# Kernel optimization log

Hardware: AMD Instinct MI355X
Metric: run time of the kernel (lower is better)

The kernel has to match this reference:

```python
import jax, jax.numpy as jnp
import numpy as np
from functools import partial

TOP_K = 2
LN_EPS = 1e-5


def setup_inputs() -> dict:
    key = jax.random.key(0)
    ks = jax.random.split(key, 4)
    B, T, H, F, E = 2, 2048, 1024, 4096, 8
    hidden_states = jax.random.normal(ks[0], (B, T, H), dtype=jnp.float32)
    # Router weights: original inits to zeros; use small random so routing is non-degenerate.
    router_w = jax.random.normal(ks[1], (E, H), dtype=jnp.float32) * 0.02
    router_b = jnp.zeros((E,), dtype=jnp.float32)
    W1 = jax.random.normal(ks[2], (E, H, F), dtype=jnp.float32) * (1.0 / np.sqrt(H))
    b1 = jnp.zeros((E, F), dtype=jnp.float32)
    W2 = jax.random.normal(ks[3], (E, F, H), dtype=jnp.float32) * (1.0 / np.sqrt(F))
    b2 = jnp.zeros((E, H), dtype=jnp.float32)
    ln_gamma = jnp.ones((H,), dtype=jnp.float32)
    ln_beta = jnp.zeros((H,), dtype=jnp.float32)
    return {"hidden_states": hidden_states, "router_w": router_w, "router_b": router_b,
            "W1": W1, "b1": b1, "W2": W2, "b2": b2,
            "ln_gamma": ln_gamma, "ln_beta": ln_beta}


def _layer_norm(x, gamma, beta):
    mu = jnp.mean(x, axis=-1, keepdims=True)
    var = jnp.var(x, axis=-1, keepdims=True)
    return (x - mu) * jax.lax.rsqrt(var + LN_EPS) * gamma + beta


def _moe_forward(hidden_states, router_w, router_b, W1, b1, W2, b2, ln_gamma, ln_beta):
    B, T, H = hidden_states.shape
    E = router_w.shape[0]
    N = B * T
    x = hidden_states.reshape(N, H)
    # Router (jitter=0.0, eval mode): logits [N, E]
    logits = x @ router_w.T + router_b
    topk_vals, topk_idx = jax.lax.top_k(logits, TOP_K)        # [N, K]
    topk_w = jax.nn.softmax(topk_vals, axis=-1)               # [N, K]
    # Scatter top-k weights into a dense combine matrix [N, E] (zeros elsewhere).
    probs = jnp.zeros((N, E), dtype=x.dtype).at[jnp.arange(N)[:, None], topk_idx].set(topk_w)
    # Per-expert FFN via scan over the (small, fixed) expert axis; each step is one
    # big GEMM over all tokens weighted by that expert's combine prob (0 for
    # tokens not routed to it) — same math as gather/MLP/scatter with no capacity drop.
    def body(acc, params_e):
        Wa, ba, Wb, bb, pe = params_e          # pe: [N]
        h = jax.nn.gelu(x @ Wa + ba, approximate=False)   # [N, F]
        y = h @ Wb + bb                                    # [N, H]
        return acc + y * pe[:, None], None
    out, _ = jax.lax.scan(body, jnp.zeros_like(x), (W1, b1, W2, b2, probs.T))
    out = out.reshape(B, T, H)
    return _layer_norm(out + hidden_states, ln_gamma, ln_beta)


def reference(hidden_states, router_w, router_b, W1, b1, W2, b2, ln_gamma, ln_beta):
    return _moe_forward(hidden_states, router_w, router_b, W1, b1, W2, b2, ln_gamma, ln_beta)
```

## Files before the change

kernel.cpp:

```cpp
#include <hip/hip_runtime.h>
#include <hip/hip_bf16.h>


typedef unsigned short u16;
typedef unsigned int u32;
typedef __attribute__((ext_vector_type(4))) float f32x4;
typedef __attribute__((ext_vector_type(8))) short s16x8;
typedef __attribute__((ext_vector_type(8))) unsigned short u16x8;

#define GLD16(gp, lp) __builtin_amdgcn_global_load_lds( \
    (const __attribute__((address_space(1))) void*)(gp), \
    (__attribute__((address_space(3))) void*)(lp), 16, 0, 0)

__device__ __forceinline__ u16 f2bf(float f) {
    union { float f; u32 u; } v; v.f = f;
    u32 u = v.u;
    return (u16)((u + 0x7fffu + ((u >> 16) & 1u)) >> 16);
}

__device__ __forceinline__ float gelu_f(float v) {
    const float u = v * (0.7978845608f + 0.0356774081f * v * v);
    const float t = __expf(-2.0f * u);
    return v * __builtin_amdgcn_rcpf(1.0f + t);
}

__global__ void k_init(int* cc) { if (threadIdx.x < 16) cc[threadIdx.x] = 0; }

__global__ __launch_bounds__(256) void k_router(
    const float* __restrict__ x, const float* __restrict__ rw, const float* __restrict__ rb,
    u16* __restrict__ xb, int* __restrict__ eidx, float* __restrict__ wgt, int* __restrict__ counts)
{
    const int wav = threadIdx.x >> 6, lane = threadIdx.x & 63;
    const int t = blockIdx.x * 4 + wav;
    const float* xt = x + (size_t)t * 1024;
    float acc[8] = {0.f,0.f,0.f,0.f,0.f,0.f,0.f,0.f};
    #pragma unroll
    for (int c = 0; c < 4; c++) {
        const int base = c * 256 + lane * 4;
        const float4 xv = *(const float4*)(xt + base);
        ushort4 pk;
        pk.x = f2bf(xv.x); pk.y = f2bf(xv.y); pk.z = f2bf(xv.z); pk.w = f2bf(xv.w);
        *(ushort4*)(xb + (size_t)t * 1024 + base) = pk;
        #pragma unroll
        for (int e = 0; e < 8; e++) {
            const float4 wv = *(const float4*)(rw + e * 1024 + base);
            acc[e] += xv.x * wv.x + xv.y * wv.y + xv.z * wv.z + xv.w * wv.w;
        }
    }
    #pragma unroll
    for (int e = 0; e < 8; e++) {
        #pragma unroll
        for (int s = 32; s; s >>= 1) acc[e] += __shfl_xor(acc[e], s);
    }
    if (lane == 0) {
        float v0 = -3e38f, v1 = -3e38f; int i0 = 0, i1 = 0;
        #pragma unroll
        for (int e = 0; e < 8; e++) {
            const float l = acc[e] + rb[e];
            if (l > v0) { v1 = v0; i1 = i0; v0 = l; i0 = e; }
            else if (l > v1) { v1 = l; i1 = e; }
        }
        const float w0 = 1.0f / (1.0f + expf(v1 - v0));
        eidx[2 * t] = i0; eidx[2 * t + 1] = i1;
        wgt[2 * t] = w0; wgt[2 * t + 1] = 1.0f - w0;
        atomicAdd(&counts[i0], 1); atomicAdd(&counts[i1], 1);
    }
}

__global__ void k_offsets(const int* __restrict__ counts, int* __restrict__ offsets) {
    if (threadIdx.x == 0) {
        int s = 0;
        for (int e = 0; e < 8; e++) { offsets[e] = s; s += counts[e]; }
        offsets[8] = s;
    }
}

__global__ __launch_bounds__(256) void k_place(
    const int* __restrict__ eidx, const int* __restrict__ offsets, int* __restrict__ cursors,
    int* __restrict__ rows, int* __restrict__ pos_of)
{
    const int a = blockIdx.x * 256 + threadIdx.x;
    const int e = eidx[a];
    const int pos = offsets[e] + atomicAdd(&cursors[e], 1);
    rows[pos] = a >> 1;
    pos_of[a] = pos;
}

__global__ __launch_bounds__(256) void k_transp(
    const float* __restrict__ src, u16* __restrict__ dst, int R, int C)
{
    const int e = blockIdx.z;
    const float* s = src + (size_t)e * R * C;
    u16* d = dst + (size_t)e * R * C;
    const int c = blockIdx.x * 64 + (threadIdx.x >> 2);
    const int r0 = blockIdx.y * 32 + (threadIdx.x & 3) * 8;
    u16x8 v;
    #pragma unroll
    for (int k = 0; k < 8; k++)
        v[k] = f2bf(s[(size_t)(r0 + k) * C + c]);
    *(u16x8*)(d + (size_t)c * R + r0) = v;
}

__global__ __launch_bounds__(256, 4) void k_gemm1(
    const u16* __restrict__ xb, const u16* __restrict__ W1t, const float* __restrict__ b1,
    u16* __restrict__ hbuf, const int* __restrict__ rows, const int* __restrict__ offsets)
{
    const int fid = blockIdx.x;
    const int swz = (fid & 7) * 1024 + (fid >> 3);
    const int y = swz & 31, xx = (swz >> 5) & 31, e = swz >> 10;

    const int off = offsets[e], cnt = offsets[e + 1] - off;
    const int row0 = y * 128;
    if (row0 >= cnt) return;
    const int n0 = xx * 128;
    const int tid = threadIdx.x;
    const int lane = tid & 63, wav = tid >> 6;

    __shared__ u16 At[2][128][32];
    __shared__ u16 Bt[2][128][32];

    const int ar0 = tid >> 2, ar1 = ar0 + 64;
    const int cl8 = (tid & 3) * 8;
    const int t0 = rows[off + min(row0 + ar0, cnt - 1)];
    const int t1 = rows[off + min(row0 + ar1, cnt - 1)];
    const u16* a_src0 = xb + (size_t)t0 * 1024 + cl8;
    const u16* a_src1 = xb + (size_t)t1 * 1024 + cl8;
    const u16* b_src0 = W1t + ((size_t)e * 4096 + n0 + ar0) * 1024 + cl8;
    const u16* b_src1 = W1t + ((size_t)e * 4096 + n0 + ar1) * 1024 + cl8;

    f32x4 acc[4][4] = {};
    const int wr = wav >> 1, wc = wav & 1;
    const int koff = (lane >> 4) * 8;
    const u16* Ab = &At[0][wr * 64 + (lane & 15)][koff];
    const u16* Bb = &Bt[0][wc * 64 + (lane & 15)][koff];

    #define STAGE1(b, k0) { \
        char* ad = (char*)At + (b) * 8192 + wav * 1024; \
        char* bd = (char*)Bt + (b) * 8192 + wav * 1024; \
        GLD16(a_src0 + (k0), ad); \
        GLD16(a_src1 + (k0), ad + 4096); \
        GLD16(b_src0 + (k0), bd); \
        GLD16(b_src1 + (k0), bd + 4096); }

    #define COMPUTE1(b) { \
        const u16* Abp = Ab + (b) * 4096; \
        const u16* Bbp = Bb + (b) * 4096; \
        s16x8 af[4], bfr[4]; \
        _Pragma("unroll") \
        for (int i = 0; i < 4; i++) { \
            af[i]  = *(const s16x8*)(Abp + i * 512); \
            bfr[i] = *(const s16x8*)(Bbp + i * 512); \
        } \
        _Pragma("unroll") \
        for (int mi = 0; mi < 4; mi++) \
            _Pragma("unroll") \
            for (int ni = 0; ni < 4; ni++) \
                acc[mi][ni] = __builtin_amdgcn_mfma_f32_16x16x32_bf16(af[mi], bfr[ni], acc[mi][ni], 0, 0, 0); }

    int b = 0;
    STAGE1(0, 0);
    __syncthreads();
    for (int k0 = 32; k0 < 1024; k0 += 32) {
        STAGE1(b ^ 1, k0);
        COMPUTE1(b);
        __syncthreads();
        b ^= 1;
    }
    COMPUTE1(b);

    const int rb4 = (lane >> 4) * 4;
    const int colbase = n0 + wc * 64 + (lane & 15);
    float bias[4];
    #pragma unroll
    for (int ni = 0; ni < 4; ni++) bias[ni] = b1[e * 4096 + colbase + ni * 16];
    #pragma unroll
    for (int mi = 0; mi < 4; mi++) {
        #pragma unroll
        for (int j = 0; j < 4; j++) {
            const int lrow = wr * 64 + mi * 16 + rb4 + j;
            if (row0 + lrow < cnt) {
                const size_t gr = (size_t)(off + row0 + lrow);
                #pragma unroll
                for (int ni = 0; ni < 4; ni++) {
                    const float v = acc[mi][ni][j] + bias[ni];
                    hbuf[gr * 4096 + colbase + ni * 16] = f2bf(gelu_f(v));
                }
            }
        }
    }
}

__global__ __launch_bounds__(256, 4) void k_gemm2(
    const u16* __restrict__ hbuf, const u16* __restrict__ W2t, const float* __restrict__ b2,
    float* __restrict__ y0, float* __restrict__ y1, const int* __restrict__ offsets)
{
    const int fid = blockIdx.x;
    const int swz = (fid & 7) * 512 + (fid >> 3);
    const int y = swz & 31, xx = (swz >> 5) & 7, z = swz >> 8;
    const int e = z >> 1, kh = z & 1;

    const int off = offsets[e], cnt = offsets[e + 1] - off;
    const int row0 = y * 128;
    if (row0 >= cnt) return;
    const int n0 = xx * 128;
    const int tid = threadIdx.x;
    const int lane = tid & 63, wav = tid >> 6;
    const int kbase = kh * 2048;

    __shared__ u16 At[2][128][32];
    __shared__ u16 Bt[2][128][32];

    const int ar0 = tid >> 2, ar1 = ar0 + 64;
    const int cl8 = (tid & 3) * 8;
    const u16* a_src0 = hbuf + (size_t)(off + min(row0 + ar0, cnt - 1)) * 4096 + kbase + cl8;
    const u16* a_src1 = hbuf + (size_t)(off + min(row0 + ar1, cnt - 1)) * 4096 + kbase + cl8;
    const u16* b_src0 = W2t + ((size_t)e * 1024 + n0 + ar0) * 4096 + kbase + cl8;
    const u16* b_src1 = W2t + ((size_t)e * 1024 + n0 + ar1) * 4096 + kbase + cl8;

    f32x4 acc[4][4] = {};
    const int wr = wav >> 1, wc = wav & 1;
    const int koff = (lane >> 4) * 8;
    const u16* Ab = &At[0][wr * 64 + (lane & 15)][koff];
    const u16* Bb = &Bt[0][wc * 64 + (lane & 15)][koff];

    int b = 0;
    STAGE1(0, 0);
    __syncthreads();
    for (int k0 = 32; k0 < 2048; k0 += 32) {
        STAGE1(b ^ 1, k0);
        COMPUTE1(b);
        __syncthreads();
        b ^= 1;
    }
    COMPUTE1(b);

    float* yy = kh ? y1 : y0;
    const int rb4 = (lane >> 4) * 4;
    const int colbase = n0 + wc * 64 + (lane & 15);
    float bias[4];
    #pragma unroll
    for (int ni = 0; ni < 4; ni++) bias[ni] = kh ? 0.f : b2[e * 1024 + colbase + ni * 16];
    #pragma unroll
    for (int mi = 0; mi < 4; mi++) {
        #pragma unroll
        for (int j = 0; j < 4; j++) {
            const int lrow = wr * 64 + mi * 16 + rb4 + j;
            if (row0 + lrow < cnt) {
                const size_t gr = (size_t)(off + row0 + lrow);
                #pragma unroll
                for (int ni = 0; ni < 4; ni++)
                    yy[gr * 1024 + colbase + ni * 16] = acc[mi][ni][j] + bias[ni];
            }
        }
    }
}

__global__ __launch_bounds__(256) void k_combine(
    const float* __restrict__ x, const float* __restrict__ y0, const float* __restrict__ y1,
    const int* __restrict__ pos_of, const float* __restrict__ wgt,
    const float* __restrict__ gamma, const float* __restrict__ beta,
    float* __restrict__ out)
{
    const int t = blockIdx.x;
    const int tid = threadIdx.x;
    const int p0 = pos_of[2 * t], p1 = pos_of[2 * t + 1];
    const float w0 = wgt[2 * t], w1 = wgt[2 * t + 1];
    const int j4 = tid * 4;
    const float4 xv = *(const float4*)(x + (size_t)t * 1024 + j4);
    const float4 ya0 = *(const float4*)(y0 + (size_t)p0 * 1024 + j4);
    const float4 yb0 = *(const float4*)(y1 + (size_t)p0 * 1024 + j4);
    const float4 ya1 = *(const float4*)(y0 + (size_t)p1 * 1024 + j4);
    const float4 yb1 = *(const float4*)(y1 + (size_t)p1 * 1024 + j4);
    float a0 = xv.x + w0 * (ya0.x + yb0.x) + w1 * (ya1.x + yb1.x);
    float a1 = xv.y + w0 * (ya0.y + yb0.y) + w1 * (ya1.y + yb1.y);
    float a2 = xv.z + w0 * (ya0.z + yb0.z) + w1 * (ya1.z + yb1.z);
    float a3 = xv.w + w0 * (ya0.w + yb0.w) + w1 * (ya1.w + yb1.w);
    float s = a0 + a1 + a2 + a3;
    float q = a0 * a0 + a1 * a1 + a2 * a2 + a3 * a3;
    #pragma unroll
    for (int o = 32; o; o >>= 1) { s += __shfl_xor(s, o); q += __shfl_xor(q, o); }
    __shared__ float ls[4], lq[4];
    const int wav = tid >> 6, lane = tid & 63;
    if (lane == 0) { ls[wav] = s; lq[wav] = q; }
    __syncthreads();
    s = ls[0] + ls[1] + ls[2] + ls[3];
    q = lq[0] + lq[1] + lq[2] + lq[3];
    const float mu = s * (1.0f / 1024.0f);
    const float var = q * (1.0f / 1024.0f) - mu * mu;
    const float rs = rsqrtf(var + 1e-5f);
    const float4 g = *(const float4*)(gamma + j4);
    const float4 b = *(const float4*)(beta + j4);
    float4 o4;
    o4.x = (a0 - mu) * rs * g.x + b.x;
    o4.y = (a1 - mu) * rs * g.y + b.y;
    o4.z = (a2 - mu) * rs * g.z + b.z;
    o4.w = (a3 - mu) * rs * g.w + b.w;
    *(float4*)(out + (size_t)t * 1024 + j4) = o4;
}

extern "C" void kernel_launch(void* const* d_in, const int* in_sizes, int n_in,
                              void* d_out, int out_size, void* d_ws, size_t ws_size,
                              hipStream_t stream) {
    const float* x     = (const float*)d_in[0];
    const float* rw    = (const float*)d_in[1];
    const float* rb    = (const float*)d_in[2];
    const float* W1    = (const float*)d_in[3];
    const float* b1    = (const float*)d_in[4];
    const float* W2    = (const float*)d_in[5];
    const float* b2    = (const float*)d_in[6];
    const float* gamma = (const float*)d_in[7];
    const float* beta  = (const float*)d_in[8];
    float* out = (float*)d_out;

    char* p = (char*)d_ws;
    auto alloc = [&](size_t bytes) { char* r = p; p += (bytes + 255) & ~(size_t)255; return r; };
    int*   counts  = (int*)alloc(16 * sizeof(int));
    int*   cursors = counts + 8;
    int*   offsets = (int*)alloc(9 * sizeof(int));
    int*   eidx    = (int*)alloc(8192 * sizeof(int));
    float* wgt     = (float*)alloc(8192 * sizeof(float));
    int*   pos_of  = (int*)alloc(8192 * sizeof(int));
    int*   rows    = (int*)alloc(8192 * sizeof(int));
    u16*   xb      = (u16*)alloc((size_t)4096 * 1024 * 2);
    u16*   W1t     = (u16*)alloc((size_t)8 * 4096 * 1024 * 2);
    u16*   W2t     = (u16*)alloc((size_t)8 * 1024 * 4096 * 2);
    u16*   hbuf    = (u16*)alloc((size_t)8192 * 4096 * 2);
    float* y0 = (float*)W1t;
    float* y1 = y0 + (size_t)8192 * 1024;

    hipLaunchKernelGGL(k_init, dim3(1), dim3(64), 0, stream, counts);
    hipLaunchKernelGGL(k_router, dim3(1024), dim3(256), 0, stream, x, rw, rb, xb, eidx, wgt, counts);
    hipLaunchKernelGGL(k_offsets, dim3(1), dim3(64), 0, stream, counts, offsets);
    hipLaunchKernelGGL(k_place, dim3(32), dim3(256), 0, stream, eidx, offsets, cursors, rows, pos_of);
    hipLaunchKernelGGL(k_transp, dim3(64, 32, 8), dim3(256), 0, stream, W1, W1t, 1024, 4096);
    hipLaunchKernelGGL(k_transp, dim3(16, 128, 8), dim3(256), 0, stream, W2, W2t, 4096, 1024);
    hipLaunchKernelGGL(k_gemm1, dim3(8192), dim3(256), 0, stream, xb, W1t, b1, hbuf, rows, offsets);
    hipLaunchKernelGGL(k_gemm2, dim3(4096), dim3(256), 0, stream, hbuf, W2t, b2, y0, y1, offsets);
    hipLaunchKernelGGL(k_combine, dim3(4096), dim3(256), 0, stream, x, y0, y1, pos_of, wgt, gamma, beta, out);
}
```

Measured before the change: 477.6 us.

## Fuse weight fp32-to-bf16 transpose into GEMM tile loads, drop transpose kernels

Removes the two standalone weight transpose/convert kernels. Each GEMM now loads fp32 weights directly, converts them to bf16 in registers and writes them transposed into padded LDS (stride 40). The A and B tiles switch from async global-to-LDS loads to register-staged loads, and occupancy drops to 3 blocks. This avoids a full pass writing and rereading the bf16 weight copies, but each GEMM tile now reads fp32 weights (twice the bytes), and those weights are re-read across the many token tiles per expert.

```diff
diff --git a/kernel.cpp b/kernel.cpp
--- a/kernel.cpp
+++ b/kernel.cpp
@@ -8,9 +8,7 @@
 typedef __attribute__((ext_vector_type(8))) short s16x8;
 typedef __attribute__((ext_vector_type(8))) unsigned short u16x8;
 
-#define GLD16(gp, lp) __builtin_amdgcn_global_load_lds( \
-    (const __attribute__((address_space(1))) void*)(gp), \
-    (__attribute__((address_space(3))) void*)(lp), 16, 0, 0)
+#define LDSTR 40
 
 __device__ __forceinline__ u16 f2bf(float f) {
     union { float f; u32 u; } v; v.f = f;
@@ -86,23 +84,8 @@
     pos_of[a] = pos;
 }
 
-__global__ __launch_bounds__(256) void k_transp(
-    const float* __restrict__ src, u16* __restrict__ dst, int R, int C)
-{
-    const int e = blockIdx.z;
-    const float* s = src + (size_t)e * R * C;
-    u16* d = dst + (size_t)e * R * C;
-    const int c = blockIdx.x * 64 + (threadIdx.x >> 2);
-    const int r0 = blockIdx.y * 32 + (threadIdx.x & 3) * 8;
-    u16x8 v;
-    #pragma unroll
-    for (int k = 0; k < 8; k++)
-        v[k] = f2bf(s[(size_t)(r0 + k) * C + c]);
-    *(u16x8*)(d + (size_t)c * R + r0) = v;
-}
-
-__global__ __launch_bounds__(256, 4) void k_gemm1(
-    const u16* __restrict__ xb, const u16* __restrict__ W1t, const float* __restrict__ b1,
+__global__ __launch_bounds__(256, 3) void k_gemm1(
+    const u16* __restrict__ xb, const float* __restrict__ W1, const float* __restrict__ b1,
     u16* __restrict__ hbuf, const int* __restrict__ rows, const int* __restrict__ offsets)
 {
     const int fid = blockIdx.x;
@@ -114,62 +97,75 @@
     if (row0 >= cnt) return;
     const int n0 = xx * 128;
     const int tid = threadIdx.x;
-    const int lane = tid & 63, wav = tid >> 6;
-
-    __shared__ u16 At[2][128][32];
-    __shared__ u16 Bt[2][128][32];
-
-    const int ar0 = tid >> 2, ar1 = ar0 + 64;
-    const int cl8 = (tid & 3) * 8;
-    const int t0 = rows[off + min(row0 + ar0, cnt - 1)];
-    const int t1 = rows[off + min(row0 + ar1, cnt - 1)];
-    const u16* a_src0 = xb + (size_t)t0 * 1024 + cl8;
-    const u16* a_src1 = xb + (size_t)t1 * 1024 + cl8;
-    const u16* b_src0 = W1t + ((size_t)e * 4096 + n0 + ar0) * 1024 + cl8;
-    const u16* b_src1 = W1t + ((size_t)e * 4096 + n0 + ar1) * 1024 + cl8;
+    const int lane = tid & 63, wav = tid >> 6, lane15 = lane & 15;
+
+    __shared__ u16 AtP[2][128][LDSTR];
+    __shared__ u16 BtP[2][128][LDSTR];
+
+    const int arow = tid >> 1, ahalf = tid & 1;
+    const int tok = rows[off + min(row0 + arow, cnt - 1)];
+    const u16* a_row = xb + (size_t)tok * 1024 + ahalf * 16;
+    const float* b_row = W1 + ((size_t)e * 1024 + wav * 8) * 4096 + n0 + lane * 2;
+
+    s16x8 aw0, aw1;
+    float2 bw[8];
+
+    auto loadA = [&](int k0) {
+        aw0 = *(const s16x8*)(a_row + k0);
+        aw1 = *(const s16x8*)(a_row + k0 + 8);
+    };
+    auto loadB = [&](int k0) {
+        #pragma unroll
+        for (int i = 0; i < 8; i++)
+            bw[i] = *(const float2*)(b_row + (size_t)(k0 + i) * 4096);
+    };
+    auto writeA = [&](int b) {
+        *(s16x8*)(&AtP[b][arow][ahalf * 16]) = aw0;
+        *(s16x8*)(&AtP[b][arow][ahalf * 16 + 8]) = aw1;
+    };
+    auto writeB = [&](int b) {
+        s16x8 v0, v1;
+        #pragma unroll
+        for (int i = 0; i < 8; i++) { v0[i] = (short)f2bf(bw[i].x); v1[i] = (short)f2bf(bw[i].y); }
+        *(s16x8*)(&BtP[b][lane * 2][wav * 8]) = v0;
+        *(s16x8*)(&BtP[b][lane * 2 + 1][wav * 8]) = v1;
+    };
 
     f32x4 acc[4][4] = {};
     const int wr = wav >> 1, wc = wav & 1;
     const int koff = (lane >> 4) * 8;
-    const u16* Ab = &At[0][wr * 64 + (lane & 15)][koff];
-    const u16* Bb = &Bt[0][wc * 64 + (lane & 15)][koff];
-
-    #define STAGE1(b, k0) { \
-        char* ad = (char*)At + (b) * 8192 + wav * 1024; \
-        char* bd = (char*)Bt + (b) * 8192 + wav * 1024; \
-        GLD16(a_src0 + (k0), ad); \
-        GLD16(a_src1 + (k0), ad + 4096); \
-        GLD16(b_src0 + (k0), bd); \
-        GLD16(b_src1 + (k0), bd + 4096); }
-
-    #define COMPUTE1(b) { \
-        const u16* Abp = Ab + (b) * 4096; \
-        const u16* Bbp = Bb + (b) * 4096; \
-        s16x8 af[4], bfr[4]; \
-        _Pragma("unroll") \
-        for (int i = 0; i < 4; i++) { \
-            af[i]  = *(const s16x8*)(Abp + i * 512); \
-            bfr[i] = *(const s16x8*)(Bbp + i * 512); \
-        } \
-        _Pragma("unroll") \
-        for (int mi = 0; mi < 4; mi++) \
-            _Pragma("unroll") \
-            for (int ni = 0; ni < 4; ni++) \
-                acc[mi][ni] = __builtin_amdgcn_mfma_f32_16x16x32_bf16(af[mi], bfr[ni], acc[mi][ni], 0, 0, 0); }
-
-    int b = 0;
-    STAGE1(0, 0);
+
+    auto compute = [&](int b) {
+        const u16* Ap = &AtP[b][wr * 64 + lane15][koff];
+        const u16* Bp = &BtP[b][wc * 64 + lane15][koff];
+        s16x8 af[4], bfr[4];
+        #pragma unroll
+        for (int i = 0; i < 4; i++) {
+            af[i]  = *(const s16x8*)(Ap + i * 16 * LDSTR);
+            bfr[i] = *(const s16x8*)(Bp + i * 16 * LDSTR);
+        }
+        #pragma unroll
+        for (int mi = 0; mi < 4; mi++)
+            #pragma unroll
+            for (int ni = 0; ni < 4; ni++)
+                acc[mi][ni] = __builtin_amdgcn_mfma_f32_16x16x32_bf16(af[mi], bfr[ni], acc[mi][ni], 0, 0, 0);
+    };
+
+    loadA(0); loadB(0);
+    writeA(0); writeB(0);
     __syncthreads();
+    int cur = 0;
     for (int k0 = 32; k0 < 1024; k0 += 32) {
-        STAGE1(b ^ 1, k0);
-        COMPUTE1(b);
+        loadA(k0); loadB(k0);
+        compute(cur);
+        writeA(cur ^ 1); writeB(cur ^ 1);
         __syncthreads();
-        b ^= 1;
-    }
-    COMPUTE1(b);
+        cur ^= 1;
+    }
+    compute(cur);
 
     const int rb4 = (lane >> 4) * 4;
-    const int colbase = n0 + wc * 64 + (lane & 15);
+    const int colbase = n0 + wc * 64 + lane15;
     float bias[4];
     #pragma unroll
     for (int ni = 0; ni < 4; ni++) bias[ni] = b1[e * 4096 + colbase + ni * 16];
@@ -190,8 +186,8 @@
     }
 }
 
-__global__ __launch_bounds__(256, 4) void k_gemm2(
-    const u16* __restrict__ hbuf, const u16* __restrict__ W2t, const float* __restrict__ b2,
+__global__ __launch_bounds__(256, 3) void k_gemm2(
+    const u16* __restrict__ hbuf, const float* __restrict__ W2, const float* __restrict__ b2,
     float* __restrict__ y0, float* __restrict__ y1, const int* __restrict__ offsets)
 {
     const int fid = blockIdx.x;
@@ -204,39 +200,76 @@
     if (row0 >= cnt) return;
     const int n0 = xx * 128;
     const int tid = threadIdx.x;
-    const int lane = tid & 63, wav = tid >> 6;
+    const int lane = tid & 63, wav = tid >> 6, lane15 = lane & 15;
     const int kbase = kh * 2048;
 
-    __shared__ u16 At[2][128][32];
-    __shared__ u16 Bt[2][128][32];
-
-    const int ar0 = tid >> 2, ar1 = ar0 + 64;
-    const int cl8 = (tid & 3) * 8;
-    const u16* a_src0 = hbuf + (size_t)(off + min(row0 + ar0, cnt - 1)) * 4096 + kbase + cl8;
-    const u16* a_src1 = hbuf + (size_t)(off + min(row0 + ar1, cnt - 1)) * 4096 + kbase + cl8;
-    const u16* b_src0 = W2t + ((size_t)e * 1024 + n0 + ar0) * 4096 + kbase + cl8;
-    const u16* b_src1 = W2t + ((size_t)e * 1024 + n0 + ar1) * 4096 + kbase + cl8;
+    __shared__ u16 AtP[2][128][LDSTR];
+    __shared__ u16 BtP[2][128][LDSTR];
+
+    const int arow = tid >> 1, ahalf = tid & 1;
+    const u16* a_row = hbuf + (size_t)(off + min(row0 + arow, cnt - 1)) * 4096 + kbase + ahalf * 16;
+    const float* b_row = W2 + ((size_t)e * 4096 + kbase + wav * 8) * 1024 + n0 + lane * 2;
+
+    s16x8 aw0, aw1;
+    float2 bw[8];
+
+    auto loadA = [&](int k0) {
+        aw0 = *(const s16x8*)(a_row + k0);
+        aw1 = *(const s16x8*)(a_row + k0 + 8);
+    };
+    auto loadB = [&](int k0) {
+        #pragma unroll
+        for (int i = 0; i < 8; i++)
+            bw[i] = *(const float2*)(b_row + (size_t)(k0 + i) * 1024);
+    };
+    auto writeA = [&](int b) {
+        *(s16x8*)(&AtP[b][arow][ahalf * 16]) = aw0;
+        *(s16x8*)(&AtP[b][arow][ahalf * 16 + 8]) = aw1;
+    };
+    auto writeB = [&](int b) {
+        s16x8 v0, v1;
+        #pragma unroll
+        for (int i = 0; i < 8; i++) { v0[i] = (short)f2bf(bw[i].x); v1[i] = (short)f2bf(bw[i].y); }
+        *(s16x8*)(&BtP[b][lane * 2][wav * 8]) = v0;
+        *(s16x8*)(&BtP[b][lane * 2 + 1][wav * 8]) = v1;
+    };
 
     f32x4 acc[4][4] = {};
     const int wr = wav >> 1, wc = wav & 1;
     const int koff = (lane >> 4) * 8;
-    const u16* Ab = &At[0][wr * 64 + (lane & 15)][koff];
-    const u16* Bb = &Bt[0][wc * 64 + (lane & 15)][koff];
-
-    int b = 0;
-    STAGE1(0, 0);
+
+    auto compute = [&](int b) {
+        const u16* Ap = &AtP[b][wr * 64 + lane15][koff];
+        const u16* Bp = &BtP[b][wc * 64 + lane15][koff];
+        s16x8 af[4], bfr[4];
+        #pragma unroll
+        for (int i = 0; i < 4; i++) {
+            af[i]  = *(const s16x8*)(Ap + i * 16 * LDSTR);
+            bfr[i] = *(const s16x8*)(Bp + i * 16 * LDSTR);
+        }
+        #pragma unroll
+        for (int mi = 0; mi < 4; mi++)
+            #pragma unroll
+            for (int ni = 0; ni < 4; ni++)
+                acc[mi][ni] = __builtin_amdgcn_mfma_f32_16x16x32_bf16(af[mi], bfr[ni], acc[mi][ni], 0, 0, 0);
+    };
+
+    loadA(0); loadB(0);
+    writeA(0); writeB(0);
     __syncthreads();
+    int cur = 0;
     for (int k0 = 32; k0 < 2048; k0 += 32) {
-        STAGE1(b ^ 1, k0);
-        COMPUTE1(b);
+        loadA(k0); loadB(k0);
+        compute(cur);
+        writeA(cur ^ 1); writeB(cur ^ 1);
         __syncthreads();
-        b ^= 1;
-    }
-    COMPUTE1(b);
+        cur ^= 1;
+    }
+    compute(cur);
 
     float* yy = kh ? y1 : y0;
     const int rb4 = (lane >> 4) * 4;
-    const int colbase = n0 + wc * 64 + (lane & 15);
+    const int colbase = n0 + wc * 64 + lane15;
     float bias[4];
     #pragma unroll
     for (int ni = 0; ni < 4; ni++) bias[ni] = kh ? 0.f : b2[e * 1024 + colbase + ni * 16];
@@ -322,19 +355,15 @@
     int*   pos_of  = (int*)alloc(8192 * sizeof(int));
     int*   rows    = (int*)alloc(8192 * sizeof(int));
     u16*   xb      = (u16*)alloc((size_t)4096 * 1024 * 2);
-    u16*   W1t     = (u16*)alloc((size_t)8 * 4096 * 1024 * 2);
-    u16*   W2t     = (u16*)alloc((size_t)8 * 1024 * 4096 * 2);
     u16*   hbuf    = (u16*)alloc((size_t)8192 * 4096 * 2);
-    float* y0 = (float*)W1t;
-    float* y1 = y0 + (size_t)8192 * 1024;
+    float* y0      = (float*)alloc((size_t)8192 * 1024 * 4);
+    float* y1      = (float*)alloc((size_t)8192 * 1024 * 4);
 
     hipLaunchKernelGGL(k_init, dim3(1), dim3(64), 0, stream, counts);
     hipLaunchKernelGGL(k_router, dim3(1024), dim3(256), 0, stream, x, rw, rb, xb, eidx, wgt, counts);
     hipLaunchKernelGGL(k_offsets, dim3(1), dim3(64), 0, stream, counts, offsets);
     hipLaunchKernelGGL(k_place, dim3(32), dim3(256), 0, stream, eidx, offsets, cursors, rows, pos_of);
-    hipLaunchKernelGGL(k_transp, dim3(64, 32, 8), dim3(256), 0, stream, W1, W1t, 1024, 4096);
-    hipLaunchKernelGGL(k_transp, dim3(16, 128, 8), dim3(256), 0, stream, W2, W2t, 4096, 1024);
-    hipLaunchKernelGGL(k_gemm1, dim3(8192), dim3(256), 0, stream, xb, W1t, b1, hbuf, rows, offsets);
-    hipLaunchKernelGGL(k_gemm2, dim3(4096), dim3(256), 0, stream, hbuf, W2t, b2, y0, y1, offsets);
+    hipLaunchKernelGGL(k_gemm1, dim3(8192), dim3(256), 0, stream, xb, W1, b1, hbuf, rows, offsets);
+    hipLaunchKernelGGL(k_gemm2, dim3(4096), dim3(256), 0, stream, hbuf, W2, b2, y0, y1, offsets);
     hipLaunchKernelGGL(k_combine, dim3(4096), dim3(256), 0, stream, x, y0, y1, pos_of, wgt, gamma, beta, out);
 }
```

After: 546.1 us. 14.3% more time.

## Make expert GEMMs persistent with per-XCD atomic tile queues; store GEMM2 outputs in bf16

Applied to the files above, without the earlier changes.

Both expert GEMM kernels become persistent grids of 1024 blocks. Each block pulls tile indices from a per-XCD atomic counter over a compact list of only the valid (expert, row-tile, col-tile) combinations. This avoids launching thousands of blocks that exit early for empty row tiles, and it keeps tiles of the same expert on the same XCD for L2 reuse. The GEMM2 partial outputs are also written as bf16 instead of fp32, which halves the write and combine-read traffic at some cost in precision.

```diff
diff --git a/kernel.cpp b/kernel.cpp
--- a/kernel.cpp
+++ b/kernel.cpp
@@ -17,6 +17,9 @@
     u32 u = v.u;
     return (u16)((u + 0x7fffu + ((u >> 16) & 1u)) >> 16);
 }
+__device__ __forceinline__ float bf2f(u16 h) {
+    union { u32 u; float f; } v; v.u = ((u32)h) << 16; return v.f;
+}
 
 __device__ __forceinline__ float gelu_f(float v) {
     const float u = v * (0.7978845608f + 0.0356774081f * v * v);
@@ -24,7 +27,7 @@
     return v * __builtin_amdgcn_rcpf(1.0f + t);
 }
 
-__global__ void k_init(int* cc) { if (threadIdx.x < 16) cc[threadIdx.x] = 0; }
+__global__ void k_init(int* cc) { if (threadIdx.x < 32) cc[threadIdx.x] = 0; }
 
 __global__ __launch_bounds__(256) void k_router(
     const float* __restrict__ x, const float* __restrict__ rw, const float* __restrict__ rb,
@@ -101,89 +104,115 @@
     *(u16x8*)(d + (size_t)c * R + r0) = v;
 }
 
+#define STAGE_T(b, k0) { \
+    char* ad = (char*)At + (b) * 8192 + wav * 1024; \
+    char* bd = (char*)Bt + (b) * 8192 + wav * 1024; \
+    GLD16(a_src0 + (k0), ad); \
+    GLD16(a_src1 + (k0), ad + 4096); \
+    GLD16(b_src0 + (k0), bd); \
+    GLD16(b_src1 + (k0), bd + 4096); }
+
+#define COMPUTE_T(b) { \
+    const u16* Abp = Ab + (b) * 4096; \
+    const u16* Bbp = Bb + (b) * 4096; \
+    s16x8 af[4], bfr[4]; \
+    _Pragma("unroll") \
+    for (int i = 0; i < 4; i++) { \
+        af[i]  = *(const s16x8*)(Abp + i * 512); \
+        bfr[i] = *(const s16x8*)(Bbp + i * 512); \
+    } \
+    _Pragma("unroll") \
+    for (int mi = 0; mi < 4; mi++) \
+        _Pragma("unroll") \
+        for (int ni = 0; ni < 4; ni++) \
+            acc[mi][ni] = __builtin_amdgcn_mfma_f32_16x16x32_bf16(af[mi], bfr[ni], acc[mi][ni], 0, 0, 0); }
+
 __global__ __launch_bounds__(256, 4) void k_gemm1(
     const u16* __restrict__ xb, const u16* __restrict__ W1t, const float* __restrict__ b1,
-    u16* __restrict__ hbuf, const int* __restrict__ rows, const int* __restrict__ offsets)
-{
-    const int fid = blockIdx.x;
-    const int swz = (fid & 7) * 1024 + (fid >> 3);
-    const int y = swz & 31, xx = (swz >> 5) & 31, e = swz >> 10;
-
-    const int off = offsets[e], cnt = offsets[e + 1] - off;
-    const int row0 = y * 128;
-    if (row0 >= cnt) return;
-    const int n0 = xx * 128;
+    u16* __restrict__ hbuf, const int* __restrict__ rows, const int* __restrict__ offsets,
+    int* __restrict__ wk)
+{
     const int tid = threadIdx.x;
     const int lane = tid & 63, wav = tid >> 6;
+    const int xcd = blockIdx.x & 7;
+
+    int base_e[9], rt_e[8];
+    int T = 0;
+    #pragma unroll
+    for (int e = 0; e < 8; e++) {
+        base_e[e] = T;
+        const int c = offsets[e + 1] - offsets[e];
+        rt_e[e] = (c + 127) >> 7;
+        T += rt_e[e] * 32;
+    }
+    base_e[8] = T;
+    const int Tx = (T + 7) >> 3;
+    const int tbeg = xcd * Tx, tend = min(T, tbeg + Tx);
 
     __shared__ u16 At[2][128][32];
     __shared__ u16 Bt[2][128][32];
-
-    const int ar0 = tid >> 2, ar1 = ar0 + 64;
-    const int cl8 = (tid & 3) * 8;
-    const int t0 = rows[off + min(row0 + ar0, cnt - 1)];
-    const int t1 = rows[off + min(row0 + ar1, cnt - 1)];
-    const u16* a_src0 = xb + (size_t)t0 * 1024 + cl8;
-    const u16* a_src1 = xb + (size_t)t1 * 1024 + cl8;
-    const u16* b_src0 = W1t + ((size_t)e * 4096 + n0 + ar0) * 1024 + cl8;
-    const u16* b_src1 = W1t + ((size_t)e * 4096 + n0 + ar1) * 1024 + cl8;
-
-    f32x4 acc[4][4] = {};
+    __shared__ int s_t;
+
     const int wr = wav >> 1, wc = wav & 1;
+    const int lane15 = lane & 15;
     const int koff = (lane >> 4) * 8;
-    const u16* Ab = &At[0][wr * 64 + (lane & 15)][koff];
-    const u16* Bb = &Bt[0][wc * 64 + (lane & 15)][koff];
-
-    #define STAGE1(b, k0) { \
-        char* ad = (char*)At + (b) * 8192 + wav * 1024; \
-        char* bd = (char*)Bt + (b) * 8192 + wav * 1024; \
-        GLD16(a_src0 + (k0), ad); \
-        GLD16(a_src1 + (k0), ad + 4096); \
-        GLD16(b_src0 + (k0), bd); \
-        GLD16(b_src1 + (k0), bd + 4096); }
-
-    #define COMPUTE1(b) { \
-        const u16* Abp = Ab + (b) * 4096; \
-        const u16* Bbp = Bb + (b) * 4096; \
-        s16x8 af[4], bfr[4]; \
-        _Pragma("unroll") \
-        for (int i = 0; i < 4; i++) { \
-            af[i]  = *(const s16x8*)(Abp + i * 512); \
-            bfr[i] = *(const s16x8*)(Bbp + i * 512); \
-        } \
-        _Pragma("unroll") \
-        for (int mi = 0; mi < 4; mi++) \
-            _Pragma("unroll") \
-            for (int ni = 0; ni < 4; ni++) \
-                acc[mi][ni] = __builtin_amdgcn_mfma_f32_16x16x32_bf16(af[mi], bfr[ni], acc[mi][ni], 0, 0, 0); }
-
-    int b = 0;
-    STAGE1(0, 0);
-    __syncthreads();
-    for (int k0 = 32; k0 < 1024; k0 += 32) {
-        STAGE1(b ^ 1, k0);
-        COMPUTE1(b);
-        __syncthreads();
-        b ^= 1;
-    }
-    COMPUTE1(b);
-
-    const int rb4 = (lane >> 4) * 4;
-    const int colbase = n0 + wc * 64 + (lane & 15);
-    float bias[4];
-    #pragma unroll
-    for (int ni = 0; ni < 4; ni++) bias[ni] = b1[e * 4096 + colbase + ni * 16];
-    #pragma unroll
-    for (int mi = 0; mi < 4; mi++) {
-        #pragma unroll
-        for (int j = 0; j < 4; j++) {
-            const int lrow = wr * 64 + mi * 16 + rb4 + j;
-            if (row0 + lrow < cnt) {
-                const size_t gr = (size_t)(off + row0 + lrow);
-                #pragma unroll
-                for (int ni = 0; ni < 4; ni++) {
-                    const float v = acc[mi][ni][j] + bias[ni];
-                    hbuf[gr * 4096 + colbase + ni * 16] = f2bf(gelu_f(v));
+    const int ar0 = tid >> 2, cl8 = (tid & 3) * 8;
+    const u16* Ab = &At[0][wr * 64 + lane15][koff];
+    const u16* Bb = &Bt[0][wc * 64 + lane15][koff];
+
+    for (;;) {
+        __syncthreads();
+        if (tid == 0) s_t = atomicAdd(&wk[xcd], 1);
+        __syncthreads();
+        const int t = tbeg + s_t;
+        if (t >= tend) break;
+
+        int e = 0;
+        #pragma unroll
+        for (int q = 0; q < 7; q++) if (t >= base_e[q + 1]) e = q + 1;
+        const int idx = t - base_e[e];
+        const int rte = rt_e[e];
+        const int nt = idx / rte, rt = idx - nt * rte;
+
+        const int off = offsets[e], cnt = offsets[e + 1] - off;
+        const int row0 = rt * 128, n0 = nt * 128;
+
+        const int t0 = rows[off + min(row0 + ar0, cnt - 1)];
+        const int t1 = rows[off + min(row0 + ar0 + 64, cnt - 1)];
+        const u16* a_src0 = xb + (size_t)t0 * 1024 + cl8;
+        const u16* a_src1 = xb + (size_t)t1 * 1024 + cl8;
+        const u16* b_src0 = W1t + ((size_t)e * 4096 + n0 + ar0) * 1024 + cl8;
+        const u16* b_src1 = b_src0 + (size_t)64 * 1024;
+
+        f32x4 acc[4][4] = {};
+        STAGE_T(0, 0);
+        __syncthreads();
+        int b = 0;
+        for (int k0 = 32; k0 < 1024; k0 += 32) {
+            STAGE_T(b ^ 1, k0);
+            COMPUTE_T(b);
+            __syncthreads();
+            b ^= 1;
+        }
+        COMPUTE_T(b);
+
+        const int rb4 = (lane >> 4) * 4;
+        const int colbase = n0 + wc * 64 + lane15;
+        float bias[4];
+        #pragma unroll
+        for (int ni = 0; ni < 4; ni++) bias[ni] = b1[e * 4096 + colbase + ni * 16];
+        #pragma unroll
+        for (int mi = 0; mi < 4; mi++) {
+            #pragma unroll
+            for (int j = 0; j < 4; j++) {
+                const int lrow = wr * 64 + mi * 16 + rb4 + j;
+                if (row0 + lrow < cnt) {
+                    const size_t gr = (size_t)(off + row0 + lrow);
+                    #pragma unroll
+                    for (int ni = 0; ni < 4; ni++) {
+                        const float v = acc[mi][ni][j] + bias[ni];
+                        hbuf[gr * 4096 + colbase + ni * 16] = f2bf(gelu_f(v));
+                    }
                 }
             }
         }
@@ -192,71 +221,97 @@
 
 __global__ __launch_bounds__(256, 4) void k_gemm2(
     const u16* __restrict__ hbuf, const u16* __restrict__ W2t, const float* __restrict__ b2,
-    float* __restrict__ y0, float* __restrict__ y1, const int* __restrict__ offsets)
-{
-    const int fid = blockIdx.x;
-    const int swz = (fid & 7) * 512 + (fid >> 3);
-    const int y = swz & 31, xx = (swz >> 5) & 7, z = swz >> 8;
-    const int e = z >> 1, kh = z & 1;
-
-    const int off = offsets[e], cnt = offsets[e + 1] - off;
-    const int row0 = y * 128;
-    if (row0 >= cnt) return;
-    const int n0 = xx * 128;
+    u16* __restrict__ y0b, u16* __restrict__ y1b, const int* __restrict__ offsets,
+    int* __restrict__ wk)
+{
     const int tid = threadIdx.x;
     const int lane = tid & 63, wav = tid >> 6;
-    const int kbase = kh * 2048;
+    const int xcd = blockIdx.x & 7;
+
+    int base_e[9], rt_e[8];
+    int T = 0;
+    #pragma unroll
+    for (int e = 0; e < 8; e++) {
+        base_e[e] = T;
+        const int c = offsets[e + 1] - offsets[e];
+        rt_e[e] = (c + 127) >> 7;
+        T += rt_e[e] * 16;
+    }
+    base_e[8] = T;
+    const int Tx = (T + 7) >> 3;
+    const int tbeg = xcd * Tx, tend = min(T, tbeg + Tx);
 
     __shared__ u16 At[2][128][32];
     __shared__ u16 Bt[2][128][32];
-
-    const int ar0 = tid >> 2, ar1 = ar0 + 64;
-    const int cl8 = (tid & 3) * 8;
-    const u16* a_src0 = hbuf + (size_t)(off + min(row0 + ar0, cnt - 1)) * 4096 + kbase + cl8;
-    const u16* a_src1 = hbuf + (size_t)(off + min(row0 + ar1, cnt - 1)) * 4096 + kbase + cl8;
-    const u16* b_src0 = W2t + ((size_t)e * 1024 + n0 + ar0) * 4096 + kbase + cl8;
-    const u16* b_src1 = W2t + ((size_t)e * 1024 + n0 + ar1) * 4096 + kbase + cl8;
-
-    f32x4 acc[4][4] = {};
+    __shared__ int s_t;
+
     const int wr = wav >> 1, wc = wav & 1;
+    const int lane15 = lane & 15;
     const int koff = (lane >> 4) * 8;
-    const u16* Ab = &At[0][wr * 64 + (lane & 15)][koff];
-    const u16* Bb = &Bt[0][wc * 64 + (lane & 15)][koff];
-
-    int b = 0;
-    STAGE1(0, 0);
-    __syncthreads();
-    for (int k0 = 32; k0 < 2048; k0 += 32) {
-        STAGE1(b ^ 1, k0);
-        COMPUTE1(b);
-        __syncthreads();
-        b ^= 1;
-    }
-    COMPUTE1(b);
-
-    float* yy = kh ? y1 : y0;
-    const int rb4 = (lane >> 4) * 4;
-    const int colbase = n0 + wc * 64 + (lane & 15);
-    float bias[4];
-    #pragma unroll
-    for (int ni = 0; ni < 4; ni++) bias[ni] = kh ? 0.f : b2[e * 1024 + colbase + ni * 16];
-    #pragma unroll
-    for (int mi = 0; mi < 4; mi++) {
-        #pragma unroll
-        for (int j = 0; j < 4; j++) {
-            const int lrow = wr * 64 + mi * 16 + rb4 + j;
-            if (row0 + lrow < cnt) {
-                const size_t gr = (size_t)(off + row0 + lrow);
-                #pragma unroll
-                for (int ni = 0; ni < 4; ni++)
-                    yy[gr * 1024 + colbase + ni * 16] = acc[mi][ni][j] + bias[ni];
+    const int ar0 = tid >> 2, cl8 = (tid & 3) * 8;
+    const u16* Ab = &At[0][wr * 64 + lane15][koff];
+    const u16* Bb = &Bt[0][wc * 64 + lane15][koff];
+
+    for (;;) {
+        __syncthreads();
+        if (tid == 0) s_t = atomicAdd(&wk[xcd], 1);
+        __syncthreads();
+        const int t = tbeg + s_t;
+        if (t >= tend) break;
+
+        int e = 0;
+        #pragma unroll
+        for (int q = 0; q < 7; q++) if (t >= base_e[q + 1]) e = q + 1;
+        const int idx = t - base_e[e];
+        const int rte = rt_e[e];
+        const int nk = idx / rte, rt = idx - nk * rte;
+        const int nt = nk >> 1, kh = nk & 1;
+
+        const int off = offsets[e], cnt = offsets[e + 1] - off;
+        const int row0 = rt * 128, n0 = nt * 128;
+        const int kbase = kh * 2048;
+
+        const u16* a_src0 = hbuf + (size_t)(off + min(row0 + ar0, cnt - 1)) * 4096 + kbase + cl8;
+        const u16* a_src1 = hbuf + (size_t)(off + min(row0 + ar0 + 64, cnt - 1)) * 4096 + kbase + cl8;
+        const u16* b_src0 = W2t + ((size_t)e * 1024 + n0 + ar0) * 4096 + kbase + cl8;
+        const u16* b_src1 = b_src0 + (size_t)64 * 4096;
+
+        f32x4 acc[4][4] = {};
+        STAGE_T(0, 0);
+        __syncthreads();
+        int b = 0;
+        for (int k0 = 32; k0 < 2048; k0 += 32) {
+            STAGE_T(b ^ 1, k0);
+            COMPUTE_T(b);
+            __syncthreads();
+            b ^= 1;
+        }
+        COMPUTE_T(b);
+
+        u16* yy = kh ? y1b : y0b;
+        const int rb4 = (lane >> 4) * 4;
+        const int colbase = n0 + wc * 64 + lane15;
+        float bias[4];
+        #pragma unroll
+        for (int ni = 0; ni < 4; ni++) bias[ni] = kh ? 0.f : b2[e * 1024 + colbase + ni * 16];
+        #pragma unroll
+        for (int mi = 0; mi < 4; mi++) {
+            #pragma unroll
+            for (int j = 0; j < 4; j++) {
+                const int lrow = wr * 64 + mi * 16 + rb4 + j;
+                if (row0 + lrow < cnt) {
+                    const size_t gr = (size_t)(off + row0 + lrow);
+                    #pragma unroll
+                    for (int ni = 0; ni < 4; ni++)
+                        yy[gr * 1024 + colbase + ni * 16] = f2bf(acc[mi][ni][j] + bias[ni]);
+                }
             }
         }
     }
 }
 
 __global__ __launch_bounds__(256) void k_combine(
-    const float* __restrict__ x, const float* __restrict__ y0, const float* __restrict__ y1,
+    const float* __restrict__ x, const u16* __restrict__ y0b, const u16* __restrict__ y1b,
     const int* __restrict__ pos_of, const float* __restrict__ wgt,
     const float* __restrict__ gamma, const float* __restrict__ beta,
     float* __restrict__ out)
@@ -267,14 +322,14 @@
     const float w0 = wgt[2 * t], w1 = wgt[2 * t + 1];
     const int j4 = tid * 4;
     const float4 xv = *(const float4*)(x + (size_t)t * 1024 + j4);
-    const float4 ya0 = *(const float4*)(y0 + (size_t)p0 * 1024 + j4);
-    const float4 yb0 = *(const float4*)(y1 + (size_t)p0 * 1024 + j4);
-    const float4 ya1 = *(const float4*)(y0 + (size_t)p1 * 1024 + j4);
-    const float4 yb1 = *(const float4*)(y1 + (size_t)p1 * 1024 + j4);
-    float a0 = xv.x + w0 * (ya0.x + yb0.x) + w1 * (ya1.x + yb1.x);
-    float a1 = xv.y + w0 * (ya0.y + yb0.y) + w1 * (ya1.y + yb1.y);
-    float a2 = xv.z + w0 * (ya0.z + yb0.z) + w1 * (ya1.z + yb1.z);
-    float a3 = xv.w + w0 * (ya0.w + yb0.w) + w1 * (ya1.w + yb1.w);
+    const ushort4 ua0 = *(const ushort4*)(y0b + (size_t)p0 * 1024 + j4);
+    const ushort4 ub0 = *(const ushort4*)(y1b + (size_t)p0 * 1024 + j4);
+    const ushort4 ua1 = *(const ushort4*)(y0b + (size_t)p1 * 1024 + j4);
+    const ushort4 ub1 = *(const ushort4*)(y1b + (size_t)p1 * 1024 + j4);
+    float a0 = xv.x + w0 * (bf2f(ua0.x) + bf2f(ub0.x)) + w1 * (bf2f(ua1.x) + bf2f(ub1.x));
+    float a1 = xv.y + w0 * (bf2f(ua0.y) + bf2f(ub0.y)) + w1 * (bf2f(ua1.y) + bf2f(ub1.y));
+    float a2 = xv.z + w0 * (bf2f(ua0.z) + bf2f(ub0.z)) + w1 * (bf2f(ua1.z) + bf2f(ub1.z));
+    float a3 = xv.w + w0 * (bf2f(ua0.w) + bf2f(ub0.w)) + w1 * (bf2f(ua1.w) + bf2f(ub1.w));
     float s = a0 + a1 + a2 + a3;
     float q = a0 * a0 + a1 * a1 + a2 * a2 + a3 * a3;
     #pragma unroll
@@ -314,8 +369,11 @@
 
     char* p = (char*)d_ws;
     auto alloc = [&](size_t bytes) { char* r = p; p += (bytes + 255) & ~(size_t)255; return r; };
-    int*   counts  = (int*)alloc(16 * sizeof(int));
-    int*   cursors = counts + 8;
+    int*   ctrl    = (int*)alloc(32 * sizeof(int));
+    int*   counts  = ctrl;
+    int*   cursors = ctrl + 8;
+    int*   g1cur   = ctrl + 16;
+    int*   g2cur   = ctrl + 24;
     int*   offsets = (int*)alloc(9 * sizeof(int));
     int*   eidx    = (int*)alloc(8192 * sizeof(int));
     float* wgt     = (float*)alloc(8192 * sizeof(float));
@@ -325,16 +383,16 @@
     u16*   W1t     = (u16*)alloc((size_t)8 * 4096 * 1024 * 2);
     u16*   W2t     = (u16*)alloc((size_t)8 * 1024 * 4096 * 2);
     u16*   hbuf    = (u16*)alloc((size_t)8192 * 4096 * 2);
-    float* y0 = (float*)W1t;
-    float* y1 = y0 + (size_t)8192 * 1024;
-
-    hipLaunchKernelGGL(k_init, dim3(1), dim3(64), 0, stream, counts);
+    u16* y0b = W1t;
+    u16* y1b = W1t + (size_t)8192 * 1024;
+
+    hipLaunchKernelGGL(k_init, dim3(1), dim3(64), 0, stream, ctrl);
     hipLaunchKernelGGL(k_router, dim3(1024), dim3(256), 0, stream, x, rw, rb, xb, eidx, wgt, counts);
     hipLaunchKernelGGL(k_offsets, dim3(1), dim3(64), 0, stream, counts, offsets);
     hipLaunchKernelGGL(k_place, dim3(32), dim3(256), 0, stream, eidx, offsets, cursors, rows, pos_of);
     hipLaunchKernelGGL(k_transp, dim3(64, 32, 8), dim3(256), 0, stream, W1, W1t, 1024, 4096);
     hipLaunchKernelGGL(k_transp, dim3(16, 128, 8), dim3(256), 0, stream, W2, W2t, 4096, 1024);
-    hipLaunchKernelGGL(k_gemm1, dim3(8192), dim3(256), 0, stream, xb, W1t, b1, hbuf, rows, offsets);
-    hipLaunchKernelGGL(k_gemm2, dim3(4096), dim3(256), 0, stream, hbuf, W2t, b2, y0, y1, offsets);
-    hipLaunchKernelGGL(k_combine, dim3(4096), dim3(256), 0, stream, x, y0, y1, pos_of, wgt, gamma, beta, out);
-}
+    hipLaunchKernelGGL(k_gemm1, dim3(1024), dim3(256), 0, stream, xb, W1t, b1, hbuf, rows, offsets, g1cur);
+    hipLaunchKernelGGL(k_gemm2, dim3(1024), dim3(256), 0, stream, hbuf, W2t, b2, y0b, y1b, offsets, g2cur);
+    hipLaunchKernelGGL(k_combine, dim3(4096), dim3(256), 0, stream, x, y0b, y1b, pos_of, wgt, gamma, beta, out);
+}
```

Measured after the change: 519.9 us. 1.09x slower.

## Swizzle LDS tiles, use explicit vmcnt waits, setprio MFMA, store bf16 outputs

Applied to the files above, without the earlier changes.

XOR-swizzles the k-chunk placement in LDS for both expert GEMMs so fragment reads avoid bank conflicts. Replaces __syncthreads with explicit vmcnt waits plus barriers so the next tile's loads stay in flight during compute. Raises wave priority around the MFMA block. GEMM2 partial outputs are now stored as bf16 instead of fp32 to halve combine traffic, at some precision cost.

```diff
diff --git a/kernel.cpp b/kernel.cpp
--- a/kernel.cpp
+++ b/kernel.cpp
@@ -16,6 +16,9 @@
     union { float f; u32 u; } v; v.f = f;
     u32 u = v.u;
     return (u16)((u + 0x7fffu + ((u >> 16) & 1u)) >> 16);
+}
+__device__ __forceinline__ float bf2f(u16 h) {
+    union { u32 u; float f; } v; v.u = ((u32)h) << 16; return v.f;
 }
 
 __device__ __forceinline__ float gelu_f(float v) {
@@ -101,6 +104,35 @@
     *(u16x8*)(d + (size_t)c * R + r0) = v;
 }
 
+#define STAGE_T(b, k0) { \
+    char* ad = (char*)At + (b) * 8192 + wav * 1024; \
+    char* bd = (char*)Bt + (b) * 8192 + wav * 1024; \
+    GLD16(a_src0 + (k0), ad); \
+    GLD16(a_src1 + (k0), ad + 4096); \
+    GLD16(b_src0 + (k0), bd); \
+    GLD16(b_src1 + (k0), bd + 4096); }
+
+#define COMPUTE_T(b) { \
+    const u16* Abp = Ab + (b) * 4096; \
+    const u16* Bbp = Bb + (b) * 4096; \
+    s16x8 af[4], bfr[4]; \
+    _Pragma("unroll") \
+    for (int i = 0; i < 4; i++) { \
+        af[i]  = *(const s16x8*)(Abp + i * 512); \
+        bfr[i] = *(const s16x8*)(Bbp + i * 512); \
+    } \
+    __builtin_amdgcn_s_setprio(1); \
+    _Pragma("unroll") \
+    for (int mi = 0; mi < 4; mi++) \
+        _Pragma("unroll") \
+        for (int ni = 0; ni < 4; ni++) \
+            acc[mi][ni] = __builtin_amdgcn_mfma_f32_16x16x32_bf16(af[mi], bfr[ni], acc[mi][ni], 0, 0, 0); \
+    __builtin_amdgcn_s_setprio(0); }
+
+#define VMCNT4 asm volatile("s_waitcnt vmcnt(4)" ::: "memory")
+#define VMCNT0 asm volatile("s_waitcnt vmcnt(0)" ::: "memory")
+#define BAR __builtin_amdgcn_s_barrier()
+
 __global__ __launch_bounds__(256, 4) void k_gemm1(
     const u16* __restrict__ xb, const u16* __restrict__ W1t, const float* __restrict__ b1,
     u16* __restrict__ hbuf, const int* __restrict__ rows, const int* __restrict__ offsets)
@@ -114,62 +146,42 @@
     if (row0 >= cnt) return;
     const int n0 = xx * 128;
     const int tid = threadIdx.x;
-    const int lane = tid & 63, wav = tid >> 6;
+    const int lane = tid & 63, wav = tid >> 6, lane15 = lane & 15;
 
     __shared__ u16 At[2][128][32];
     __shared__ u16 Bt[2][128][32];
 
-    const int ar0 = tid >> 2, ar1 = ar0 + 64;
-    const int cl8 = (tid & 3) * 8;
+    const int ar0 = tid >> 2;
+    const int cl8 = (((tid & 3) ^ ((tid >> 3) & 3))) * 8;
     const int t0 = rows[off + min(row0 + ar0, cnt - 1)];
-    const int t1 = rows[off + min(row0 + ar1, cnt - 1)];
+    const int t1 = rows[off + min(row0 + ar0 + 64, cnt - 1)];
     const u16* a_src0 = xb + (size_t)t0 * 1024 + cl8;
     const u16* a_src1 = xb + (size_t)t1 * 1024 + cl8;
     const u16* b_src0 = W1t + ((size_t)e * 4096 + n0 + ar0) * 1024 + cl8;
-    const u16* b_src1 = W1t + ((size_t)e * 4096 + n0 + ar1) * 1024 + cl8;
+    const u16* b_src1 = b_src0 + (size_t)64 * 1024;
 
     f32x4 acc[4][4] = {};
     const int wr = wav >> 1, wc = wav & 1;
-    const int koff = (lane >> 4) * 8;
-    const u16* Ab = &At[0][wr * 64 + (lane & 15)][koff];
-    const u16* Bb = &Bt[0][wc * 64 + (lane & 15)][koff];
-
-    #define STAGE1(b, k0) { \
-        char* ad = (char*)At + (b) * 8192 + wav * 1024; \
-        char* bd = (char*)Bt + (b) * 8192 + wav * 1024; \
-        GLD16(a_src0 + (k0), ad); \
-        GLD16(a_src1 + (k0), ad + 4096); \
-        GLD16(b_src0 + (k0), bd); \
-        GLD16(b_src1 + (k0), bd + 4096); }
-
-    #define COMPUTE1(b) { \
-        const u16* Abp = Ab + (b) * 4096; \
-        const u16* Bbp = Bb + (b) * 4096; \
-        s16x8 af[4], bfr[4]; \
-        _Pragma("unroll") \
-        for (int i = 0; i < 4; i++) { \
-            af[i]  = *(const s16x8*)(Abp + i * 512); \
-            bfr[i] = *(const s16x8*)(Bbp + i * 512); \
-        } \
-        _Pragma("unroll") \
-        for (int mi = 0; mi < 4; mi++) \
-            _Pragma("unroll") \
-            for (int ni = 0; ni < 4; ni++) \
-                acc[mi][ni] = __builtin_amdgcn_mfma_f32_16x16x32_bf16(af[mi], bfr[ni], acc[mi][ni], 0, 0, 0); }
-
+    const int koff = ((lane >> 4) ^ ((lane >> 1) & 3)) * 8;
+    const u16* Ab = &At[0][wr * 64 + lane15][koff];
+    const u16* Bb = &Bt[0][wc * 64 + lane15][koff];
+
+    STAGE_T(0, 0);
     int b = 0;
-    STAGE1(0, 0);
-    __syncthreads();
     for (int k0 = 32; k0 < 1024; k0 += 32) {
-        STAGE1(b ^ 1, k0);
-        COMPUTE1(b);
-        __syncthreads();
+        STAGE_T(b ^ 1, k0);
+        VMCNT4;
+        BAR;
+        COMPUTE_T(b);
+        BAR;
         b ^= 1;
     }
-    COMPUTE1(b);
+    VMCNT0;
+    BAR;
+    COMPUTE_T(b);
 
     const int rb4 = (lane >> 4) * 4;
-    const int colbase = n0 + wc * 64 + (lane & 15);
+    const int colbase = n0 + wc * 64 + lane15;
     float bias[4];
     #pragma unroll
     for (int ni = 0; ni < 4; ni++) bias[ni] = b1[e * 4096 + colbase + ni * 16];
@@ -192,7 +204,7 @@
 
 __global__ __launch_bounds__(256, 4) void k_gemm2(
     const u16* __restrict__ hbuf, const u16* __restrict__ W2t, const float* __restrict__ b2,
-    float* __restrict__ y0, float* __restrict__ y1, const int* __restrict__ offsets)
+    u16* __restrict__ y0b, u16* __restrict__ y1b, const int* __restrict__ offsets)
 {
     const int fid = blockIdx.x;
     const int swz = (fid & 7) * 512 + (fid >> 3);
@@ -204,39 +216,42 @@
     if (row0 >= cnt) return;
     const int n0 = xx * 128;
     const int tid = threadIdx.x;
-    const int lane = tid & 63, wav = tid >> 6;
+    const int lane = tid & 63, wav = tid >> 6, lane15 = lane & 15;
     const int kbase = kh * 2048;
 
     __shared__ u16 At[2][128][32];
     __shared__ u16 Bt[2][128][32];
 
-    const int ar0 = tid >> 2, ar1 = ar0 + 64;
-    const int cl8 = (tid & 3) * 8;
+    const int ar0 = tid >> 2;
+    const int cl8 = (((tid & 3) ^ ((tid >> 3) & 3))) * 8;
     const u16* a_src0 = hbuf + (size_t)(off + min(row0 + ar0, cnt - 1)) * 4096 + kbase + cl8;
-    const u16* a_src1 = hbuf + (size_t)(off + min(row0 + ar1, cnt - 1)) * 4096 + kbase + cl8;
+    const u16* a_src1 = hbuf + (size_t)(off + min(row0 + ar0 + 64, cnt - 1)) * 4096 + kbase + cl8;
     const u16* b_src0 = W2t + ((size_t)e * 1024 + n0 + ar0) * 4096 + kbase + cl8;
-    const u16* b_src1 = W2t + ((size_t)e * 1024 + n0 + ar1) * 4096 + kbase + cl8;
+    const u16* b_src1 = b_src0 + (size_t)64 * 4096;
 
     f32x4 acc[4][4] = {};
     const int wr = wav >> 1, wc = wav & 1;
-    const int koff = (lane >> 4) * 8;
-    const u16* Ab = &At[0][wr * 64 + (lane & 15)][koff];
-    const u16* Bb = &Bt[0][wc * 64 + (lane & 15)][koff];
-
+    const int koff = ((lane >> 4) ^ ((lane >> 1) & 3)) * 8;
+    const u16* Ab = &At[0][wr * 64 + lane15][koff];
+    const u16* Bb = &Bt[0][wc * 64 + lane15][koff];
+
+    STAGE_T(0, 0);
     int b = 0;
-    STAGE1(0, 0);
-    __syncthreads();
     for (int k0 = 32; k0 < 2048; k0 += 32) {
-        STAGE1(b ^ 1, k0);
-        COMPUTE1(b);
-        __syncthreads();
+        STAGE_T(b ^ 1, k0);
+        VMCNT4;
+        BAR;
+        COMPUTE_T(b);
+        BAR;
         b ^= 1;
     }
-    COMPUTE1(b);
-
-    float* yy = kh ? y1 : y0;
+    VMCNT0;
+    BAR;
+    COMPUTE_T(b);
+
+    u16* yy = kh ? y1b : y0b;
     const int rb4 = (lane >> 4) * 4;
-    const int colbase = n0 + wc * 64 + (lane & 15);
+    const int colbase = n0 + wc * 64 + lane15;
     float bias[4];
     #pragma unroll
     for (int ni = 0; ni < 4; ni++) bias[ni] = kh ? 0.f : b2[e * 1024 + colbase + ni * 16];
@@ -249,14 +264,14 @@
                 const size_t gr = (size_t)(off + row0 + lrow);
                 #pragma unroll
                 for (int ni = 0; ni < 4; ni++)
-                    yy[gr * 1024 + colbase + ni * 16] = acc[mi][ni][j] + bias[ni];
+                    yy[gr * 1024 + colbase + ni * 16] = f2bf(acc[mi][ni][j] + bias[ni]);
             }
         }
     }
 }
 
 __global__ __launch_bounds__(256) void k_combine(
-    const float* __restrict__ x, const float* __restrict__ y0, const float* __restrict__ y1,
+    const float* __restrict__ x, const u16* __restrict__ y0b, const u16* __restrict__ y1b,
     const int* __restrict__ pos_of, const float* __restrict__ wgt,
     const float* __restrict__ gamma, const float* __restrict__ beta,
     float* __restrict__ out)
@@ -267,14 +282,14 @@
     const float w0 = wgt[2 * t], w1 = wgt[2 * t + 1];
     const int j4 = tid * 4;
     const float4 xv = *(const float4*)(x + (size_t)t * 1024 + j4);
-    const float4 ya0 = *(const float4*)(y0 + (size_t)p0 * 1024 + j4);
-    const float4 yb0 = *(const float4*)(y1 + (size_t)p0 * 1024 + j4);
-    const float4 ya1 = *(const float4*)(y0 + (size_t)p1 * 1024 + j4);
-    const float4 yb1 = *(const float4*)(y1 + (size_t)p1 * 1024 + j4);
-    float a0 = xv.x + w0 * (ya0.x + yb0.x) + w1 * (ya1.x + yb1.x);
-    float a1 = xv.y + w0 * (ya0.y + yb0.y) + w1 * (ya1.y + yb1.y);
-    float a2 = xv.z + w0 * (ya0.z + yb0.z) + w1 * (ya1.z + yb1.z);
-    float a3 = xv.w + w0 * (ya0.w + yb0.w) + w1 * (ya1.w + yb1.w);
+    const ushort4 ua0 = *(const ushort4*)(y0b + (size_t)p0 * 1024 + j4);
+    const ushort4 ub0 = *(const ushort4*)(y1b + (size_t)p0 * 1024 + j4);
+    const ushort4 ua1 = *(const ushort4*)(y0b + (size_t)p1 * 1024 + j4);
+    const ushort4 ub1 = *(const ushort4*)(y1b + (size_t)p1 * 1024 + j4);
+    float a0 = xv.x + w0 * (bf2f(ua0.x) + bf2f(ub0.x)) + w1 * (bf2f(ua1.x) + bf2f(ub1.x));
+    float a1 = xv.y + w0 * (bf2f(ua0.y) + bf2f(ub0.y)) + w1 * (bf2f(ua1.y) + bf2f(ub1.y));
+    float a2 = xv.z + w0 * (bf2f(ua0.z) + bf2f(ub0.z)) + w1 * (bf2f(ua1.z) + bf2f(ub1.z));
+    float a3 = xv.w + w0 * (bf2f(ua0.w) + bf2f(ub0.w)) + w1 * (bf2f(ua1.w) + bf2f(ub1.w));
     float s = a0 + a1 + a2 + a3;
     float q = a0 * a0 + a1 * a1 + a2 * a2 + a3 * a3;
     #pragma unroll
@@ -325,8 +340,8 @@
     u16*   W1t     = (u16*)alloc((size_t)8 * 4096 * 1024 * 2);
     u16*   W2t     = (u16*)alloc((size_t)8 * 1024 * 4096 * 2);
     u16*   hbuf    = (u16*)alloc((size_t)8192 * 4096 * 2);
-    float* y0 = (float*)W1t;
-    float* y1 = y0 + (size_t)8192 * 1024;
+    u16* y0b = W1t;
+    u16* y1b = W1t + (size_t)8192 * 1024;
 
     hipLaunchKernelGGL(k_init, dim3(1), dim3(64), 0, stream, counts);
     hipLaunchKernelGGL(k_router, dim3(1024), dim3(256), 0, stream, x, rw, rb, xb, eidx, wgt, counts);
@@ -335,6 +350,6 @@
     hipLaunchKernelGGL(k_transp, dim3(64, 32, 8), dim3(256), 0, stream, W1, W1t, 1024, 4096);
     hipLaunchKernelGGL(k_transp, dim3(16, 128, 8), dim3(256), 0, stream, W2, W2t, 4096, 1024);
     hipLaunchKernelGGL(k_gemm1, dim3(8192), dim3(256), 0, stream, xb, W1t, b1, hbuf, rows, offsets);
-    hipLaunchKernelGGL(k_gemm2, dim3(4096), dim3(256), 0, stream, hbuf, W2t, b2, y0, y1, offsets);
-    hipLaunchKernelGGL(k_combine, dim3(4096), dim3(256), 0, stream, x, y0, y1, pos_of, wgt, gamma, beta, out);
-}
+    hipLaunchKernelGGL(k_gemm2, dim3(4096), dim3(256), 0, stream, hbuf, W2t, b2, y0b, y1b, offsets);
+    hipLaunchKernelGGL(k_combine, dim3(4096), dim3(256), 0, stream, x, y0b, y1b, pos_of, wgt, gamma, beta, out);
+}
```

Result: faster. 460.5 us (-3.6%).
